# Optimization experiments

Measured on AMD Instinct MI355X. Metric: run time of the kernel, lower is better.

## Reference

```python
import jax, jax.numpy as jnp
import numpy as np

FEATURE_SCALE = 0.25  # cfg.feature_scale
G = 4                 # deformable/offset groups
K = 3                 # deform kernel size
KK = K * K
PAD = 1


def conv2d(x, w, b=None):
    y = jax.lax.conv_general_dilated(x, w, (1, 1), ((PAD, PAD), (PAD, PAD)),
                                     dimension_numbers=('NCHW', 'OIHW', 'NCHW'))
    return y if b is None else y + b[None, :, None, None]


def bilinear_upsample_ac(x, fs):
    # F.interpolate(mode='bilinear', align_corners=True, scale_factor=fs)
    b, c, H, W = x.shape
    Ho, Wo = H * fs, W * fs
    sy = jnp.arange(Ho, dtype=x.dtype) * ((H - 1) / (Ho - 1))
    sx = jnp.arange(Wo, dtype=x.dtype) * ((W - 1) / (Wo - 1))
    y0 = jnp.clip(jnp.floor(sy).astype(jnp.int32), 0, H - 2)
    x0 = jnp.clip(jnp.floor(sx).astype(jnp.int32), 0, W - 2)
    wy = (sy - y0)[None, None, :, None]
    wx = (sx - x0)[None, None, None, :]
    rows = x[:, :, y0, :] * (1 - wy) + x[:, :, y0 + 1, :] * wy
    return rows[:, :, :, x0] * (1 - wx) + rows[:, :, :, x0 + 1] * wx


def deform_conv(x, offset, mask, w):
    # torchvision.ops.deform_conv2d, stride 1, pad 1, weight groups = 1,
    # offset/mask groups = G. offset layout: (b, G*KK*2, H, W), (dy, dx) pairs.
    b, C, H, W = x.shape
    Cg = C // G
    off = offset.reshape(b, G, KK, 2, H, W)
    ii = (jnp.arange(KK) // K).reshape(1, 1, KK, 1, 1).astype(x.dtype)
    jj = (jnp.arange(KK) % K).reshape(1, 1, KK, 1, 1).astype(x.dtype)
    ys = jnp.arange(H, dtype=x.dtype).reshape(1, 1, 1, H, 1)
    xs = jnp.arange(W, dtype=x.dtype).reshape(1, 1, 1, 1, W)
    py = ys - PAD + ii + off[:, :, :, 0]   # (b,G,KK,H,W)
    px = xs - PAD + jj + off[:, :, :, 1]
    xt = x.reshape(b, G, Cg, H, W).transpose(0, 1, 3, 4, 2)  # (b,G,H,W,Cg)
    y0f = jnp.floor(py)
    x0f = jnp.floor(px)
    wy = py - y0f
    wx = px - x0f
    y0 = y0f.astype(jnp.int32)
    x0 = x0f.astype(jnp.int32)
    bi = jnp.arange(b).reshape(b, 1, 1, 1, 1)
    gi = jnp.arange(G).reshape(1, G, 1, 1, 1)

    def corner(yi, xi, wgt):
        valid = ((yi >= 0) & (yi < H) & (xi >= 0) & (xi < W)).astype(x.dtype)
        v = xt[bi, gi, jnp.clip(yi, 0, H - 1), jnp.clip(xi, 0, W - 1)]  # (b,G,KK,H,W,Cg)
        return v * (wgt * valid)[..., None]

    s = (corner(y0, x0, (1 - wy) * (1 - wx)) + corner(y0, x0 + 1, (1 - wy) * wx)
         + corner(y0 + 1, x0, wy * (1 - wx)) + corner(y0 + 1, x0 + 1, wy * wx))
    s = s * mask.reshape(b, G, KK, H, W)[..., None]
    wr = w.reshape(w.shape[0], G, Cg, KK)
    return jnp.einsum('bgkhwc,ogck->bohw', s, wr)


def _align(sou_list, ref_list, params):
    cat_feat, offset_vs = [], []
    for i in (3, 2, 1):
        sou, ref = sou_list[i - 1], ref_list[i - 1]
        b, C, H, W = sou.shape
        Cg = C // G
        off_w, off_b, mod_w, mod_b, reg_w = params[i]
        off_in = jnp.concatenate([sou.reshape(b, G, Cg, H, W),
                                  ref.reshape(b, G, Cg, H, W)], axis=2)
        off_in = off_in.reshape(b * G, 2 * Cg, H, W)
        offset = conv2d(off_in, off_w, off_b).reshape(b, G * 2 * KK, H, W)
        rng = min(H, W) * 0.5 / 2
        offset_map = rng * 2 * jax.nn.sigmoid(offset) - rng
        modulator = 2.0 * jax.nn.sigmoid(conv2d(sou, mod_w, mod_b))
        feat = deform_conv(sou, offset_map, modulator, reg_w)
        fs = int(1 // (FEATURE_SCALE / 2 ** (i - 1)))
        oy = jnp.mean(offset_map[:, 0::2], axis=1, keepdims=True)
        ox = jnp.mean(offset_map[:, 1::2], axis=1, keepdims=True)
        ov = bilinear_upsample_ac(jnp.concatenate([oy, ox], axis=1), fs) * fs
        cat_feat.append(feat)
        offset_vs.append(ov)
    return tuple(cat_feat) + tuple(offset_vs)


def setup_inputs() -> dict:
    key = jax.random.key(0)
    ks = jax.random.split(key, 32)
    d = {}
    shapes = {1: (2, 64, 128, 128), 2: (2, 64, 64, 64), 3: (2, 64, 32, 32)}
    k = 0
    for i in (1, 2, 3):
        d[f'sou{i}'] = jax.random.normal(ks[k], shapes[i], jnp.float32); k += 1
        d[f'ref{i}'] = jax.random.normal(ks[k], shapes[i], jnp.float32); k += 1
    Cg = 64 // G
    for i in (1, 2, 3):
        d[f'off_w{i}'] = jax.random.normal(ks[k], (2 * KK, 2 * Cg, K, K), jnp.float32) * 0.05; k += 1
        d[f'off_b{i}'] = jax.random.normal(ks[k], (2 * KK,), jnp.float32) * 0.05; k += 1
        d[f'mod_w{i}'] = jax.random.normal(ks[k], (G * KK, 64, K, K), jnp.float32) * 0.05; k += 1
        d[f'mod_b{i}'] = jax.random.normal(ks[k], (G * KK,), jnp.float32) * 0.05; k += 1
        d[f'reg_w{i}'] = jax.random.normal(ks[k], (64, 64, K, K), jnp.float32) * 0.05; k += 1
    return d


def reference(sou1, sou2, sou3, ref1, ref2, ref3,
              off_w1, off_b1, mod_w1, mod_b1, reg_w1,
              off_w2, off_b2, mod_w2, mod_b2, reg_w2,
              off_w3, off_b3, mod_w3, mod_b3, reg_w3):
    params = {1: (off_w1, off_b1, mod_w1, mod_b1, reg_w1),
              2: (off_w2, off_b2, mod_w2, mod_b2, reg_w2),
              3: (off_w3, off_b3, mod_w3, mod_b3, reg_w3)}
    return _align([sou1, sou2, sou3], [ref1, ref2, ref3], params)
```

## Files before the change

### kernel.cpp

```cpp
#include <hip/hip_runtime.h>

typedef __attribute__((ext_vector_type(8))) short short8;
typedef __attribute__((ext_vector_type(4))) float f32x4;

__device__ __forceinline__ float sigmoidf_(float x) { return 1.f / (1.f + __expf(-x)); }
__device__ __forceinline__ unsigned bf16rne(float x) {
    unsigned b = __float_as_uint(x);
    return (b + 0x7FFFu + ((b >> 16) & 1u)) >> 16;
}


struct P {
    const float *sou0, *sou1, *sou2;
    const float *ref0, *ref1, *ref2;
    const float *ob0, *ob1, *ob2;
    const float *mb0, *mb1, *mb2;
    float* out;
    float* ws;
};

union U {
    uint4 u4; int4 i4; short8 s8; f32x4 f4;
};

__global__ __launch_bounds__(256) void repack_all(
    const float* __restrict__ ow0, const float* __restrict__ mw0, const float* __restrict__ rw0,
    const float* __restrict__ ow1, const float* __restrict__ mw1, const float* __restrict__ rw1,
    const float* __restrict__ ow2, const float* __restrict__ mw2, const float* __restrict__ rw2,
    float* __restrict__ dst) {
    const int lvl = blockIdx.y;
    const float* ow = lvl == 0 ? ow0 : (lvl == 1 ? ow1 : ow2);
    const float* mw = lvl == 0 ? mw0 : (lvl == 1 ? mw1 : mw2);
    const float* rw = lvl == 0 ? rw0 : (lvl == 1 ? rw1 : rw2);
    unsigned* d = (unsigned*)(dst + lvl * 62784);
    int i = blockIdx.x * 256 + threadIdx.x;
    if (i < 18432) {
        int jw = i & 3;
        int lane = (i >> 2) & 63;
        int t3 = i >> 8;
        int ks = t3 % 18, wvu = t3 / 18;
        int o = wvu * 16 + (lane & 15);
        int c0 = ks * 32 + (lane >> 4) * 8 + 2 * jw;
        int g0 = c0 / 144, r0 = c0 % 144;
        int c1 = c0 + 1;
        int g1 = c1 / 144, r1 = c1 % 144;
        float w0 = rw[o * 576 + (g0 * 16 + (r0 & 15)) * 9 + (r0 >> 4)];
        float w1 = rw[o * 576 + (g1 * 16 + (r1 & 15)) * 9 + (r1 >> 4)];
        d[i] = bf16rne(w0) | (bf16rne(w1) << 16);
    } else if (i < 23040) {
        int o2 = i - 18432;
        int jw = o2 & 3;
        int lane = (o2 >> 2) & 63;
        int t2 = o2 >> 8;
        int tap = t2 >> 1, nt = t2 & 1;
        int n = nt * 16 + (lane & 15);
        int ic0 = (lane >> 4) * 8 + 2 * jw;
        float w0 = (n < 18) ? ow[n * 288 + ic0 * 9 + tap] : 0.f;
        float w1 = (n < 18) ? ow[n * 288 + (ic0 + 1) * 9 + tap] : 0.f;
        d[36864 + o2] = bf16rne(w0) | (bf16rne(w1) << 16);
    } else if (i < 36864) {
        int o3 = i - 23040;
        int jw = o3 & 3;
        int lane = (o3 >> 2) & 63;
        int t3 = o3 >> 8;
        int nt = t3 % 3, tc = t3 / 3;
        int tap = tc >> 1, c = tc & 1;
        int n = nt * 16 + (lane & 15);
        int ic0 = c * 32 + (lane >> 4) * 8 + 2 * jw;
        float w0 = (n < 36) ? mw[n * 576 + ic0 * 9 + tap] : 0.f;
        float w1 = (n < 36) ? mw[n * 576 + (ic0 + 1) * 9 + tap] : 0.f;
        d[41472 + o3] = bf16rne(w0) | (bf16rne(w1) << 16);
    }
}

__global__ __launch_bounds__(256) void k1_prep(P p) {
    __shared__ __align__(16) char smem[28512];
    const int t = blockIdx.x;
    float* ws = p.ws;
    const int tid = threadIdx.x;

    if (t < 2688) {
        int lvl, j;
        if (t < 2048) { lvl = 0; j = t; }
        else if (t < 2560) { lvl = 1; j = t - 2048; }
        else { lvl = 2; j = t - 2560; }
        const int logW = 7 - lvl;
        const int W = 1 << logW, H = W, HW = H * W;
        const int nper = 256 >> (2 * lvl);
        const int qb = j % nper, g = (j / nper) & 3, b = j / (nper * 4);
        const int q0 = qb * 64;
        const int hlo = q0 >> logW;
        const int xlo = q0 & (W - 1);
        const int cols = (W >= 64) ? 66 : 34;
        const int rcTot = (W >= 64) ? 198 : 136;
        const float* sou = lvl == 0 ? p.sou0 : (lvl == 1 ? p.sou1 : p.sou2);
        const float* ref = lvl == 0 ? p.ref0 : (lvl == 1 ? p.ref1 : p.ref2);
        const float* bases = sou + (size_t)(b * 64 + g * 16) * HW;
        const float* baser = ref + (size_t)(b * 64 + g * 16) * HW;
        unsigned* ldsW = (unsigned*)smem;
        const bool sact = tid < rcTot;
        const int srow = tid / cols, scol = tid - srow * cols;
        const int grow = hlo - 1 + srow, gcol = xlo - 1 + scol;
        const bool inb = sact && grow >= 0 && grow < H && gcol >= 0 && gcol < W;
        const size_t goff = inb ? ((size_t)grow * W + gcol) : 0;
#pragma unroll
        for (int ic = 0; ic < 32; ic += 2) {
            float v0 = 0.f, v1 = 0.f;
            if (inb) {
                const float* p0 = (ic < 16) ? bases + (size_t)ic * HW
                                            : baser + (size_t)(ic - 16) * HW;
                v0 = p0[goff]; v1 = p0[HW + goff];
            }
            if (sact) ldsW[tid * 20 + (ic >> 1)] = bf16rne(v0) | (bf16rne(v1) << 16);
        }
        __syncthreads();
        const int wvu = __builtin_amdgcn_readfirstlane(tid >> 6);
        const int lane = tid & 63, quad = lane >> 4, lo16 = lane & 15;
        const int qg = q0 + wvu * 16 + lo16;
        const int rowB = (qg >> logW) - hlo;
        const int colB = (qg & (W - 1)) - xlo;
        const unsigned short* ldsS = (const unsigned short*)smem;
        const unsigned* WBO = (const unsigned*)(ws + 4730880 + lvl * 62784) + 36864;
        f32x4 acc[2];
        acc[0] = (f32x4){0.f, 0.f, 0.f, 0.f};
        acc[1] = (f32x4){0.f, 0.f, 0.f, 0.f};
#pragma unroll
        for (int tap = 0; tap < 9; ++tap) {
            const int ky = tap / 3, kx = tap - ky * 3;
            const int rc = (rowB + ky) * cols + colB + kx;
            U au; au.s8 = *(const short8*)&ldsS[rc * 40 + quad * 8];
#pragma unroll
            for (int nt = 0; nt < 2; ++nt) {
                U bu; bu.u4 = *(const uint4*)(WBO + ((tap * 2 + nt) * 64 + lane) * 4);
                acc[nt] = __builtin_amdgcn_mfma_f32_16x16x32_bf16(au.s8, bu.s8, acc[nt], 0, 0, 0);
            }
        }
        const float* bias = lvl == 0 ? p.ob0 : (lvl == 1 ? p.ob1 : p.ob2);
        float* OFFM = ws + (lvl == 0 ? 0 : (lvl == 1 ? 2359296 : 2949120));
        const float rng = 0.25f * (float)H;
#pragma unroll
        for (int nt = 0; nt < 2; ++nt) {
            const int o = nt * 16 + lo16;
            if (o < 18) {
                const float bb = bias[o];
                float* op = OFFM + (size_t)(b * 72 + g * 18 + o) * HW + q0 + wvu * 16 + quad * 4;
#pragma unroll
                for (int rg = 0; rg < 4; ++rg)
                    op[rg] = rng * (2.f * sigmoidf_(acc[nt][rg] + bb) - 1.f);
            }
        }
    } else if (t < 3360) {
        const int i1 = t - 2688;
        int lvl, j;
        if (i1 < 512) { lvl = 0; j = i1; }
        else if (i1 < 640) { lvl = 1; j = i1 - 512; }
        else { lvl = 2; j = i1 - 640; }
        const int logW = 7 - lvl;
        const int W = 1 << logW, H = W, HW = H * W;
        const int nper = 256 >> (2 * lvl);
        const int qb = j % nper, b = j / nper;
        const int q0 = qb * 64;
        const int hlo = q0 >> logW;
        const int xlo = q0 & (W - 1);
        const int cols = (W >= 64) ? 66 : 34;
        const int rcTot = (W >= 64) ? 198 : 136;
        const float* sou = lvl == 0 ? p.sou0 : (lvl == 1 ? p.sou1 : p.sou2);
        const float* base = sou + (size_t)b * 64 * HW;
        unsigned* ldsW = (unsigned*)smem;
        const bool sact = tid < rcTot;
        const int srow = tid / cols, scol = tid - srow * cols;
        const int grow = hlo - 1 + srow, gcol = xlo - 1 + scol;
        const bool inb = sact && grow >= 0 && grow < H && gcol >= 0 && gcol < W;
        const size_t goff = inb ? ((size_t)grow * W + gcol) : 0;
#pragma unroll
        for (int ic = 0; ic < 64; ic += 2) {
            float v0 = 0.f, v1 = 0.f;
            if (inb) {
                const float* p0 = base + (size_t)ic * HW;
                v0 = p0[goff]; v1 = p0[HW + goff];
            }
            if (sact) ldsW[tid * 36 + (ic >> 1)] = bf16rne(v0) | (bf16rne(v1) << 16);
        }
        __syncthreads();
        const int wvu = __builtin_amdgcn_readfirstlane(tid >> 6);
        const int lane = tid & 63, quad = lane >> 4, lo16 = lane & 15;
        const int qg = q0 + wvu * 16 + lo16;
        const int rowB = (qg >> logW) - hlo;
        const int colB = (qg & (W - 1)) - xlo;
        const unsigned short* ldsS = (const unsigned short*)smem;
        const unsigned* WBM = (const unsigned*)(ws + 4730880 + lvl * 62784) + 41472;
        f32x4 acc[3];
        acc[0] = (f32x4){0.f, 0.f, 0.f, 0.f};
        acc[1] = (f32x4){0.f, 0.f, 0.f, 0.f};
        acc[2] = (f32x4){0.f, 0.f, 0.f, 0.f};
#pragma unroll
        for (int tap = 0; tap < 9; ++tap) {
            const int ky = tap / 3, kx = tap - ky * 3;
            const int rc = (rowB + ky) * cols + colB + kx;
#pragma unroll
            for (int c = 0; c < 2; ++c) {
                U au; au.s8 = *(const short8*)&ldsS[rc * 72 + c * 32 + quad * 8];
#pragma unroll
                for (int nt = 0; nt < 3; ++nt) {
                    U bu;
                    bu.u4 = *(const uint4*)(WBM + (((tap * 2 + c) * 3 + nt) * 64 + lane) * 4);
                    acc[nt] = __builtin_amdgcn_mfma_f32_16x16x32_bf16(au.s8, bu.s8, acc[nt], 0, 0, 0);
                }
            }
        }
        const float* bias = lvl == 0 ? p.mb0 : (lvl == 1 ? p.mb1 : p.mb2);
        float* MOD = ws + (lvl == 0 ? 3096576 : (lvl == 1 ? 4276224 : 4571136));
#pragma unroll
        for (int nt = 0; nt < 3; ++nt) {
            const int o = nt * 16 + lo16;
            if (o < 36) {
                const float bb = bias[o];
                float* op = MOD + (size_t)(b * 36 + o) * HW + q0 + wvu * 16 + quad * 4;
#pragma unroll
                for (int rg = 0; rg < 4; ++rg)
                    op[rg] = 2.f * sigmoidf_(acc[nt][rg] + bb);
            }
        }
    } else {
        const int i2 = t - 3360;
        int lvl, j;
        if (i2 < 512) { lvl = 0; j = i2; }
        else if (i2 < 640) { lvl = 1; j = i2 - 512; }
        else { lvl = 2; j = i2 - 640; }
        const int HW = 16384 >> (2 * lvl);
        const int nper = 64 >> (2 * lvl);
        const int qb = j % nper, g = (j / nper) & 3, b = j / (nper * 4);
        const float* sou = lvl == 0 ? p.sou0 : (lvl == 1 ? p.sou1 : p.sou2);
        unsigned* XTb = (unsigned*)(ws + 4919232) +
                        (lvl == 0 ? 0 : (lvl == 1 ? 1048576 : 1310720));
        float (*tile)[17] = (float(*)[17])smem;
        const int q0 = qb * 256;
        const float* src = sou + (size_t)(b * 64 + g * 16) * HW + q0;
#pragma unroll
        for (int c = 0; c < 16; ++c) tile[tid][c] = src[(size_t)c * HW + tid];
        __syncthreads();
        uint4* dst = (uint4*)(XTb + ((size_t)(b * 4 + g) * HW + q0) * 8);
#pragma unroll
        for (int u = 0; u < 2; ++u) {
            int f4 = u * 256 + tid;
            int px = f4 >> 1, hf = (f4 & 1) * 8;
            uint4 w;
            w.x = bf16rne(tile[px][hf + 0]) | (bf16rne(tile[px][hf + 1]) << 16);
            w.y = bf16rne(tile[px][hf + 2]) | (bf16rne(tile[px][hf + 3]) << 16);
            w.z = bf16rne(tile[px][hf + 4]) | (bf16rne(tile[px][hf + 5]) << 16);
            w.w = bf16rne(tile[px][hf + 6]) | (bf16rne(tile[px][hf + 7]) << 16);
            dst[f4] = w;
        }
    }
}

__global__ __launch_bounds__(256) void k2_fused(P p) {
    __shared__ unsigned lds[96 * 64];
    const int t = blockIdx.x;
    float* ws = p.ws;
    const int tid = threadIdx.x;
    if (t < 672) {
        int lvl, j;
        if (t < 512) { lvl = 0; j = t; }
        else if (t < 640) { lvl = 1; j = t - 512; }
        else { lvl = 2; j = t - 640; }
        const int logW = 7 - lvl;
        const int W = 1 << logW, H = W, HW = H * W;
        const int nper = 256 >> (2 * lvl);
        const int qb = j % nper, b = j / nper;
        const int q0 = qb * 64;
        const float* OFFM = ws + (lvl == 0 ? 0 : (lvl == 1 ? 2359296 : 2949120));
        const float* MOD = ws + (lvl == 0 ? 3096576 : (lvl == 1 ? 4276224 : 4571136));
        const unsigned* XTb = (const unsigned*)(ws + 4919232) +
                              (lvl == 0 ? 0 : (lvl == 1 ? 1048576 : 1310720));
        const unsigned* WB = (const unsigned*)(ws + 4730880 + lvl * 62784);
        float* outp = p.out + (lvl == 0 ? 655360 : (lvl == 1 ? 131072 : 0));
        const int wvu = __builtin_amdgcn_readfirstlane(tid >> 6);
        const int lane = tid & 63, quad = lane >> 4, lo16 = lane & 15;
        f32x4 acc[4];
#pragma unroll
        for (int mt = 0; mt < 4; ++mt) acc[mt] = (f32x4){0.f, 0.f, 0.f, 0.f};
        for (int c = 0; c < 3; ++c) {
            if (c) __syncthreads();
#pragma unroll
            for (int it = 0; it < 3; ++it) {
                const int task = it * 256 + tid;
                const int gkl = task >> 6, px = task & 63;
                const int gk = c * 12 + gkl;
                const int g = gk / 9, k = gk - g * 9;
                const int q = q0 + px;
                const int h = q >> logW, xp = q & (W - 1);
                const int ky = k / 3, kx = k - ky * 3;
                float dy = OFFM[(size_t)(b * 72 + g * 18 + 2 * k) * HW + q];
                float dx = OFFM[(size_t)(b * 72 + g * 18 + 2 * k + 1) * HW + q];
                float m = MOD[(size_t)(b * 36 + g * 9 + k) * HW + q];
                float py = (float)(h - 1 + ky) + dy;
                float pxx = (float)(xp - 1 + kx) + dx;
                float y0f = floorf(py), x0f = floorf(pxx);
                float wy = py - y0f, wx = pxx - x0f;
                int y0 = (int)y0f, x0 = (int)x0f;
                const unsigned* xg = XTb + (size_t)(b * 4 + g) * HW * 8;
                float s[16];
#pragma unroll
                for (int cc = 0; cc < 16; ++cc) s[cc] = 0.f;
#pragma unroll
                for (int cor = 0; cor < 4; ++cor) {
                    int yy = y0 + (cor >> 1), xx = x0 + (cor & 1);
                    float cw = ((cor >> 1) ? wy : 1.f - wy) * ((cor & 1) ? wx : 1.f - wx);
                    cw = (yy >= 0 && yy < H && xx >= 0 && xx < W) ? cw * m : 0.f;
                    int yc = min(max(yy, 0), H - 1), xc = min(max(xx, 0), W - 1);
                    const uint4* cp = (const uint4*)(xg + (size_t)((yc << logW) + xc) * 8);
                    unsigned cbuf[8];
                    *(uint4*)&cbuf[0] = cp[0];
                    *(uint4*)&cbuf[4] = cp[1];
#pragma unroll
                    for (int pr = 0; pr < 8; ++pr) {
                        float lo = __uint_as_float(cbuf[pr] << 16);
                        float hi = __uint_as_float(cbuf[pr] & 0xFFFF0000u);
                        s[2 * pr] = fmaf(cw, lo, s[2 * pr]);
                        s[2 * pr + 1] = fmaf(cw, hi, s[2 * pr + 1]);
                    }
                }
#pragma unroll
                for (int pr = 0; pr < 8; ++pr)
                    lds[(gkl * 8 + pr) * 64 + px] =
                        bf16rne(s[2 * pr]) | (bf16rne(s[2 * pr + 1]) << 16);
            }
            __syncthreads();
            uint4 bfr[6];
#pragma unroll
            for (int k6 = 0; k6 < 6; ++k6)
                bfr[k6] = *(const uint4*)(WB + (((wvu * 18 + c * 6 + k6) * 64 + lane) << 2));
#pragma unroll
            for (int k6 = 0; k6 < 6; ++k6) {
                const int rb = k6 * 16 + quad * 4;
                U bu; bu.u4 = bfr[k6];
#pragma unroll
                for (int mt = 0; mt < 4; ++mt) {
                    const int px = mt * 16 + lo16;
                    U au;
                    au.i4.x = (int)lds[(rb + 0) * 64 + px];
                    au.i4.y = (int)lds[(rb + 1) * 64 + px];
                    au.i4.z = (int)lds[(rb + 2) * 64 + px];
                    au.i4.w = (int)lds[(rb + 3) * 64 + px];
                    acc[mt] = __builtin_amdgcn_mfma_f32_16x16x32_bf16(au.s8, bu.s8, acc[mt], 0, 0, 0);
                }
            }
        }
        float* op = outp + (size_t)(b * 64 + wvu * 16 + lo16) * HW + q0;
#pragma unroll
        for (int mt = 0; mt < 4; ++mt)
#pragma unroll
            for (int rg = 0; rg < 4; ++rg)
                op[mt * 16 + quad * 4 + rg] = acc[mt][rg];
    } else {
        int i = t - 672;
        int lvl, j;
        if (i < 128) { lvl = 0; j = i; }
        else if (i < 160) { lvl = 1; j = i - 128; }
        else { lvl = 2; j = i - 160; }
        const int HW = 16384 >> (2 * lvl);
        const int nper = 64 >> (2 * lvl);
        const int qb = j % nper, b = j / nper;
        const float* OFFM = ws + (lvl == 0 ? 0 : (lvl == 1 ? 2359296 : 2949120));
        float* MEAN = ws + (lvl == 0 ? 4644864 : (lvl == 1 ? 4710400 : 4726784));
        const int q = qb * 256 + tid;
        const float* pp = OFFM + (size_t)b * 72 * HW + q;
        float sy = 0.f, sx = 0.f;
#pragma unroll
        for (int u = 0; u < 36; ++u) {
            sy += pp[(size_t)(2 * u) * HW];
            sx += pp[(size_t)(2 * u + 1) * HW];
        }
        MEAN[(size_t)(b * 2) * HW + q] = sy * (1.f / 36.f);
        MEAN[(size_t)(b * 2 + 1) * HW + q] = sx * (1.f / 36.f);
    }
}

__global__ __launch_bounds__(256) void k3_up(P p) {
    float* ws = p.ws;
    int flat = ((int)blockIdx.x * 256 + (int)threadIdx.x) * 4;
    int lvl = flat >> 20;
    int r = flat & 1048575;
    int b = r >> 19, c = (r >> 18) & 1;
    int pix = r & 262143;
    int yo = pix >> 9, xo = pix & 511;
    const int H = 128 >> lvl, W = H;
    const float* MEAN = ws + (lvl == 0 ? 4644864 : (lvl == 1 ? 4710400 : 4726784));
    const float* m = MEAN + (size_t)(b * 2 + c) * H * W;
    float* o = p.out + (lvl == 0 ? 4849664 : (lvl == 1 ? 3801088 : 2752512)) +
               ((size_t)(b * 2 + c) * 512 + yo) * 512 + xo;
    const float fs = (float)(4 << lvl);
    const float sc = (float)(H - 1) * (1.f / 511.f);
    float sy = yo * sc;
    int y0 = min((int)sy, H - 2);
    float wy = sy - (float)y0;
    float rr[4];
#pragma unroll
    for (int u = 0; u < 4; ++u) {
        float sx = (float)(xo + u) * sc;
        int x0 = min((int)sx, W - 2);
        float wx = sx - (float)x0;
        float v00 = m[y0 * W + x0], v01 = m[y0 * W + x0 + 1];
        float v10 = m[(y0 + 1) * W + x0], v11 = m[(y0 + 1) * W + x0 + 1];
        float r0 = v00 * (1.f - wy) + v10 * wy;
        float r1 = v01 * (1.f - wy) + v11 * wy;
        rr[u] = (r0 * (1.f - wx) + r1 * wx) * fs;
    }
    *(float4*)o = make_float4(rr[0], rr[1], rr[2], rr[3]);
}

extern "C" void kernel_launch(void* const* d_in, const int* in_sizes, int n_in,
                              void* d_out, int out_size, void* d_ws, size_t ws_size,
                              hipStream_t stream) {
    const float* fin[21];
    for (int i = 0; i < 21; ++i) fin[i] = (const float*)d_in[i];
    P p;
    if (in_sizes[1] == in_sizes[0]) {
        p.sou0 = fin[0]; p.ref0 = fin[1];
        p.sou1 = fin[2]; p.ref1 = fin[3];
        p.sou2 = fin[4]; p.ref2 = fin[5];
    } else {
        p.sou0 = fin[0]; p.sou1 = fin[1]; p.sou2 = fin[2];
        p.ref0 = fin[3]; p.ref1 = fin[4]; p.ref2 = fin[5];
    }
    p.ob0 = fin[7]; p.mb0 = fin[9];
    p.ob1 = fin[12]; p.mb1 = fin[14];
    p.ob2 = fin[17]; p.mb2 = fin[19];
    p.out = (float*)d_out;
    p.ws = (float*)d_ws;

    repack_all<<<dim3(144, 3), 256, 0, stream>>>(
        fin[6], fin[8], fin[10], fin[11], fin[13], fin[15], fin[16], fin[18], fin[20],
        p.ws + 4730880);
    k1_prep<<<dim3(4032), 256, 0, stream>>>(p);
    k2_fused<<<dim3(840), 256, 0, stream>>>(p);
    k3_up<<<dim3(3072), 256, 0, stream>>>(p);
}
```

Before: 192.7 us.

## Halve k2 pixel tile to 32 and vectorize k1 LDS staging stores

```diff
diff --git a/kernel.cpp b/kernel.cpp
--- a/kernel.cpp
+++ b/kernel.cpp
@@ -104,14 +104,20 @@
         const bool inb = sact && grow >= 0 && grow < H && gcol >= 0 && gcol < W;
         const size_t goff = inb ? ((size_t)grow * W + gcol) : 0;
 #pragma unroll
-        for (int ic = 0; ic < 32; ic += 2) {
-            float v0 = 0.f, v1 = 0.f;
-            if (inb) {
-                const float* p0 = (ic < 16) ? bases + (size_t)ic * HW
-                                            : baser + (size_t)(ic - 16) * HW;
-                v0 = p0[goff]; v1 = p0[HW + goff];
-            }
-            if (sact) ldsW[tid * 20 + (ic >> 1)] = bf16rne(v0) | (bf16rne(v1) << 16);
+        for (int c8 = 0; c8 < 4; ++c8) {
+            const float* p0 = (c8 < 2) ? bases + (size_t)(c8 * 8) * HW
+                                       : baser + (size_t)((c8 - 2) * 8) * HW;
+            float v[8];
+#pragma unroll
+            for (int jj = 0; jj < 8; ++jj) v[jj] = inb ? p0[(size_t)jj * HW + goff] : 0.f;
+            if (sact) {
+                uint4 wv;
+                wv.x = bf16rne(v[0]) | (bf16rne(v[1]) << 16);
+                wv.y = bf16rne(v[2]) | (bf16rne(v[3]) << 16);
+                wv.z = bf16rne(v[4]) | (bf16rne(v[5]) << 16);
+                wv.w = bf16rne(v[6]) | (bf16rne(v[7]) << 16);
+                *(uint4*)&ldsW[tid * 20 + c8 * 4] = wv;
+            }
         }
         __syncthreads();
         const int wvu = __builtin_amdgcn_readfirstlane(tid >> 6);
@@ -173,13 +179,19 @@
         const bool inb = sact && grow >= 0 && grow < H && gcol >= 0 && gcol < W;
         const size_t goff = inb ? ((size_t)grow * W + gcol) : 0;
 #pragma unroll
-        for (int ic = 0; ic < 64; ic += 2) {
-            float v0 = 0.f, v1 = 0.f;
-            if (inb) {
-                const float* p0 = base + (size_t)ic * HW;
-                v0 = p0[goff]; v1 = p0[HW + goff];
-            }
-            if (sact) ldsW[tid * 36 + (ic >> 1)] = bf16rne(v0) | (bf16rne(v1) << 16);
+        for (int c8 = 0; c8 < 8; ++c8) {
+            const float* p0 = base + (size_t)(c8 * 8) * HW;
+            float v[8];
+#pragma unroll
+            for (int jj = 0; jj < 8; ++jj) v[jj] = inb ? p0[(size_t)jj * HW + goff] : 0.f;
+            if (sact) {
+                uint4 wv;
+                wv.x = bf16rne(v[0]) | (bf16rne(v[1]) << 16);
+                wv.y = bf16rne(v[2]) | (bf16rne(v[3]) << 16);
+                wv.z = bf16rne(v[4]) | (bf16rne(v[5]) << 16);
+                wv.w = bf16rne(v[6]) | (bf16rne(v[7]) << 16);
+                *(uint4*)&ldsW[tid * 36 + c8 * 4] = wv;
+            }
         }
         __syncthreads();
         const int wvu = __builtin_amdgcn_readfirstlane(tid >> 6);
@@ -255,20 +267,20 @@
 }
 
 __global__ __launch_bounds__(256) void k2_fused(P p) {
-    __shared__ unsigned lds[96 * 64];
+    __shared__ unsigned lds[96 * 33];
     const int t = blockIdx.x;
     float* ws = p.ws;
     const int tid = threadIdx.x;
-    if (t < 672) {
+    if (t < 1344) {
         int lvl, j;
-        if (t < 512) { lvl = 0; j = t; }
-        else if (t < 640) { lvl = 1; j = t - 512; }
-        else { lvl = 2; j = t - 640; }
+        if (t < 1024) { lvl = 0; j = t; }
+        else if (t < 1280) { lvl = 1; j = t - 1024; }
+        else { lvl = 2; j = t - 1280; }
         const int logW = 7 - lvl;
         const int W = 1 << logW, H = W, HW = H * W;
-        const int nper = 256 >> (2 * lvl);
+        const int nper = 512 >> (2 * lvl);
         const int qb = j % nper, b = j / nper;
-        const int q0 = qb * 64;
+        const int q0 = qb * 32;
         const float* OFFM = ws + (lvl == 0 ? 0 : (lvl == 1 ? 2359296 : 2949120));
         const float* MOD = ws + (lvl == 0 ? 3096576 : (lvl == 1 ? 4276224 : 4571136));
         const unsigned* XTb = (const unsigned*)(ws + 4919232) +
@@ -277,54 +289,56 @@
         float* outp = p.out + (lvl == 0 ? 655360 : (lvl == 1 ? 131072 : 0));
         const int wvu = __builtin_amdgcn_readfirstlane(tid >> 6);
         const int lane = tid & 63, quad = lane >> 4, lo16 = lane & 15;
-        f32x4 acc[4];
-#pragma unroll
-        for (int mt = 0; mt < 4; ++mt) acc[mt] = (f32x4){0.f, 0.f, 0.f, 0.f};
+        f32x4 acc[2];
+        acc[0] = (f32x4){0.f, 0.f, 0.f, 0.f};
+        acc[1] = (f32x4){0.f, 0.f, 0.f, 0.f};
         for (int c = 0; c < 3; ++c) {
             if (c) __syncthreads();
 #pragma unroll
-            for (int it = 0; it < 3; ++it) {
+            for (int it = 0; it < 2; ++it) {
                 const int task = it * 256 + tid;
-                const int gkl = task >> 6, px = task & 63;
-                const int gk = c * 12 + gkl;
-                const int g = gk / 9, k = gk - g * 9;
-                const int q = q0 + px;
-                const int h = q >> logW, xp = q & (W - 1);
-                const int ky = k / 3, kx = k - ky * 3;
-                float dy = OFFM[(size_t)(b * 72 + g * 18 + 2 * k) * HW + q];
-                float dx = OFFM[(size_t)(b * 72 + g * 18 + 2 * k + 1) * HW + q];
-                float m = MOD[(size_t)(b * 36 + g * 9 + k) * HW + q];
-                float py = (float)(h - 1 + ky) + dy;
-                float pxx = (float)(xp - 1 + kx) + dx;
-                float y0f = floorf(py), x0f = floorf(pxx);
-                float wy = py - y0f, wx = pxx - x0f;
-                int y0 = (int)y0f, x0 = (int)x0f;
-                const unsigned* xg = XTb + (size_t)(b * 4 + g) * HW * 8;
-                float s[16];
-#pragma unroll
-                for (int cc = 0; cc < 16; ++cc) s[cc] = 0.f;
-#pragma unroll
-                for (int cor = 0; cor < 4; ++cor) {
-                    int yy = y0 + (cor >> 1), xx = x0 + (cor & 1);
-                    float cw = ((cor >> 1) ? wy : 1.f - wy) * ((cor & 1) ? wx : 1.f - wx);
-                    cw = (yy >= 0 && yy < H && xx >= 0 && xx < W) ? cw * m : 0.f;
-                    int yc = min(max(yy, 0), H - 1), xc = min(max(xx, 0), W - 1);
-                    const uint4* cp = (const uint4*)(xg + (size_t)((yc << logW) + xc) * 8);
-                    unsigned cbuf[8];
-                    *(uint4*)&cbuf[0] = cp[0];
-                    *(uint4*)&cbuf[4] = cp[1];
-#pragma unroll
-                    for (int pr = 0; pr < 8; ++pr) {
-                        float lo = __uint_as_float(cbuf[pr] << 16);
-                        float hi = __uint_as_float(cbuf[pr] & 0xFFFF0000u);
-                        s[2 * pr] = fmaf(cw, lo, s[2 * pr]);
-                        s[2 * pr + 1] = fmaf(cw, hi, s[2 * pr + 1]);
+                if (task < 384) {
+                    const int gkl = task >> 5, px = task & 31;
+                    const int gk = c * 12 + gkl;
+                    const int g = gk / 9, k = gk - g * 9;
+                    const int q = q0 + px;
+                    const int h = q >> logW, xp = q & (W - 1);
+                    const int ky = k / 3, kx = k - ky * 3;
+                    float dy = OFFM[(size_t)(b * 72 + g * 18 + 2 * k) * HW + q];
+                    float dx = OFFM[(size_t)(b * 72 + g * 18 + 2 * k + 1) * HW + q];
+                    float m = MOD[(size_t)(b * 36 + g * 9 + k) * HW + q];
+                    float py = (float)(h - 1 + ky) + dy;
+                    float pxx = (float)(xp - 1 + kx) + dx;
+                    float y0f = floorf(py), x0f = floorf(pxx);
+                    float wy = py - y0f, wx = pxx - x0f;
+                    int y0 = (int)y0f, x0 = (int)x0f;
+                    const unsigned* xg = XTb + (size_t)(b * 4 + g) * HW * 8;
+                    float s[16];
+#pragma unroll
+                    for (int cc = 0; cc < 16; ++cc) s[cc] = 0.f;
+#pragma unroll
+                    for (int cor = 0; cor < 4; ++cor) {
+                        int yy = y0 + (cor >> 1), xx = x0 + (cor & 1);
+                        float cw = ((cor >> 1) ? wy : 1.f - wy) * ((cor & 1) ? wx : 1.f - wx);
+                        cw = (yy >= 0 && yy < H && xx >= 0 && xx < W) ? cw * m : 0.f;
+                        int yc = min(max(yy, 0), H - 1), xc = min(max(xx, 0), W - 1);
+                        const uint4* cp = (const uint4*)(xg + (size_t)((yc << logW) + xc) * 8);
+                        unsigned cbuf[8];
+                        *(uint4*)&cbuf[0] = cp[0];
+                        *(uint4*)&cbuf[4] = cp[1];
+#pragma unroll
+                        for (int pr = 0; pr < 8; ++pr) {
+                            float lo = __uint_as_float(cbuf[pr] << 16);
+                            float hi = __uint_as_float(cbuf[pr] & 0xFFFF0000u);
+                            s[2 * pr] = fmaf(cw, lo, s[2 * pr]);
+                            s[2 * pr + 1] = fmaf(cw, hi, s[2 * pr + 1]);
+                        }
                     }
+#pragma unroll
+                    for (int pr = 0; pr < 8; ++pr)
+                        lds[(gkl * 8 + pr) * 33 + px] =
+                            bf16rne(s[2 * pr]) | (bf16rne(s[2 * pr + 1]) << 16);
                 }
-#pragma unroll
-                for (int pr = 0; pr < 8; ++pr)
-                    lds[(gkl * 8 + pr) * 64 + px] =
-                        bf16rne(s[2 * pr]) | (bf16rne(s[2 * pr + 1]) << 16);
             }
             __syncthreads();
             uint4 bfr[6];
@@ -336,25 +350,25 @@
                 const int rb = k6 * 16 + quad * 4;
                 U bu; bu.u4 = bfr[k6];
 #pragma unroll
-                for (int mt = 0; mt < 4; ++mt) {
+                for (int mt = 0; mt < 2; ++mt) {
                     const int px = mt * 16 + lo16;
                     U au;
-                    au.i4.x = (int)lds[(rb + 0) * 64 + px];
-                    au.i4.y = (int)lds[(rb + 1) * 64 + px];
-                    au.i4.z = (int)lds[(rb + 2) * 64 + px];
-                    au.i4.w = (int)lds[(rb + 3) * 64 + px];
+                    au.i4.x = (int)lds[(rb + 0) * 33 + px];
+                    au.i4.y = (int)lds[(rb + 1) * 33 + px];
+                    au.i4.z = (int)lds[(rb + 2) * 33 + px];
+                    au.i4.w = (int)lds[(rb + 3) * 33 + px];
                     acc[mt] = __builtin_amdgcn_mfma_f32_16x16x32_bf16(au.s8, bu.s8, acc[mt], 0, 0, 0);
                 }
             }
         }
         float* op = outp + (size_t)(b * 64 + wvu * 16 + lo16) * HW + q0;
 #pragma unroll
-        for (int mt = 0; mt < 4; ++mt)
+        for (int mt = 0; mt < 2; ++mt)
 #pragma unroll
             for (int rg = 0; rg < 4; ++rg)
                 op[mt * 16 + quad * 4 + rg] = acc[mt][rg];
     } else {
-        int i = t - 672;
+        int i = t - 1344;
         int lvl, j;
         if (i < 128) { lvl = 0; j = i; }
         else if (i < 160) { lvl = 1; j = i - 128; }
@@ -434,6 +448,6 @@
         fin[6], fin[8], fin[10], fin[11], fin[13], fin[15], fin[16], fin[18], fin[20],
         p.ws + 4730880);
     k1_prep<<<dim3(4032), 256, 0, stream>>>(p);
-    k2_fused<<<dim3(840), 256, 0, stream>>>(p);
+    k2_fused<<<dim3(1512), 256, 0, stream>>>(p);
     k3_up<<<dim3(3072), 256, 0, stream>>>(p);
 }
```

Result: faster. 186.3 us (-3.3%).
